# Performance work log

Measured on AMD Instinct MI355X. Metric: run time of the kernel, lower is better.

## Reference

```python
import jax, jax.numpy as jnp
import numpy as np
import math

N_NODES = 50000
N_EDGES = 500000
HIDDEN = 64
N_LAYERS = 4
DELTA = 2.5
N_AGG = 6      # mean, max, min, std, var, sum
N_SCALE = 3    # identity, amplification, attenuation
EPS_BN = 1e-5


def setup_inputs() -> dict:
    key = jax.random.key(0)
    ks = jax.random.split(key, 12)
    d = HIDDEN
    L = N_LAYERS
    din_u = (N_AGG * N_SCALE + 1) * d  # 19*d: [self || scaled aggregates]
    return {
        "node_feat": jax.random.normal(ks[0], (N_NODES, d), jnp.float32),
        "edge_feat": jax.random.normal(ks[1], (N_EDGES, 4), jnp.float32),
        "edge_src": jax.random.randint(ks[2], (N_EDGES,), 0, N_NODES, jnp.int32),
        "edge_dst": jax.random.randint(ks[3], (N_EDGES,), 0, N_NODES, jnp.int32),
        "WM": jax.random.normal(ks[4], (L, 2 * d, d), jnp.float32) / math.sqrt(2 * d),
        "bM": jnp.zeros((L, d), jnp.float32),
        "WU": jax.random.normal(ks[5], (L, din_u, d), jnp.float32) / math.sqrt(din_u),
        "bU": jnp.zeros((L, d), jnp.float32),
        "gamma_t": jnp.ones((L, d), jnp.float32),
        "beta_t": jnp.zeros((L, d), jnp.float32),
        "Wmix": jax.random.normal(ks[6], (L, d, d), jnp.float32) / math.sqrt(d),
        "bmix": jnp.zeros((L, d), jnp.float32),
        "gamma_o": jnp.ones((L, d), jnp.float32),
        "beta_o": jnp.zeros((L, d), jnp.float32),
    }


def _batchnorm(x, gamma, beta):
    # BatchNorm1d in training mode: batch stats, biased variance
    mu = jnp.mean(x, axis=0)
    var = jnp.mean(jnp.square(x - mu), axis=0)
    return (x - mu) * jax.lax.rsqrt(var + EPS_BN) * gamma + beta


def _pna_layer(h, src, dst, WM, bM, WU, bU, g_t, b_t, Wmix, bmix, g_o, b_o):
    n = h.shape[0]
    # message: M([h_src || h_dst])  -> [E, d]
    msg = jnp.concatenate([h[src], h[dst]], axis=1) @ WM + bM
    deg = jax.ops.segment_sum(jnp.ones(src.shape[0], h.dtype), dst, num_segments=n)
    denom = jnp.maximum(deg, 1.0)[:, None]
    s = jax.ops.segment_sum(msg, dst, num_segments=n)
    mean = s / denom
    mean_sq = jax.ops.segment_sum(msg * msg, dst, num_segments=n) / denom
    var = jax.nn.relu(mean_sq - mean * mean)
    std = jnp.sqrt(var + 1e-30)
    has = (deg > 0)[:, None]
    mx = jnp.where(has, jax.ops.segment_max(msg, dst, num_segments=n), 0.0)
    mn = jnp.where(has, jax.ops.segment_min(msg, dst, num_segments=n), 0.0)
    agg = jnp.concatenate([mean, mx, mn, std, var, s], axis=1)  # [N, 6d]
    # degree scalers (zero-degree nodes have all-zero agg, so 0-scale is safe)
    logD = jnp.log(deg + 1.0)[:, None]
    amp = logD / DELTA
    att = jnp.where(logD > 0, DELTA / jnp.where(logD > 0, logD, 1.0), 0.0)
    h_neigh = jnp.concatenate([agg, agg * amp, agg * att], axis=1)  # [N, 18d]
    hu = jnp.concatenate([h, h_neigh], axis=1) @ WU + bU           # [N, d]
    hu = hu * (1.0 / math.sqrt(n))  # dgl graph-size norm snorm_n = 1/sqrt(N)
    hbn = _batchnorm(hu, g_t, b_t)  # tower batchnorm; dropout p=0 -> identity
    hm = jax.nn.leaky_relu(hbn @ Wmix + bmix, 0.01)
    out = hm + h  # PNAConv internal residual (in_size == out_size)
    # outer wrapper: relu(BatchNorm(layer_out)) + node_feat
    return jax.nn.relu(_batchnorm(out, g_o, b_o)) + h


def reference(node_feat, edge_feat, edge_src, edge_dst, WM, bM, WU, bU,
              gamma_t, beta_t, Wmix, bmix, gamma_o, beta_o):
    del edge_feat  # dgl PNAConv built with edge_feat_size=0: edge feats unused
    h = node_feat
    for i in range(N_LAYERS):
        h = _pna_layer(h, edge_src, edge_dst, WM[i], bM[i], WU[i], bU[i],
                       gamma_t[i], beta_t[i], Wmix[i], bmix[i],
                       gamma_o[i], beta_o[i])
    return h
```

## Files before the change

kernel.cpp:

```cpp
#include <hip/hip_runtime.h>
#include <hip/hip_bf16.h>


#define ND 50000
#define NE 500000
#define NB_SCAN ((ND + 255) / 256)
typedef __hip_bfloat16 bh;
typedef unsigned short us;
typedef __attribute__((ext_vector_type(8))) short short8;
typedef __attribute__((ext_vector_type(4))) float floatx4;
#define MFMA(a, b, c) __builtin_amdgcn_mfma_f32_16x16x32_bf16(a, b, c, 0, 0, 0)

__device__ float B2F(us u) { union { unsigned v; float f; } c; c.v = ((unsigned)u) << 16; return c.f; }
__device__ us F2B(float x) {
  union { float f; unsigned v; } c; c.f = x;
  unsigned r = c.v + 0x7fffu + ((c.v >> 16) & 1u);
  return (us)(r >> 16);
}
__device__ float LD(const void* p, size_t i, int ib) {
  return ib ? B2F(((const us*)p)[i]) : ((const float*)p)[i];
}
__device__ void SP(us* Xh, us* Xl, size_t i, float x) {
  us h = F2B(x);
  Xh[i] = h;
  Xl[i] = F2B(x - B2F(h));
}

__device__ inline void gll16(const void* g, void* l) {
  __builtin_amdgcn_global_load_lds((const __attribute__((address_space(1))) unsigned*)g,
                                   (__attribute__((address_space(3))) unsigned*)l, 16, 0, 0);
}

__global__ void kdt(const unsigned* nf, int* fl) {
  __shared__ int cnt;
  if (threadIdx.x == 0) cnt = 0;
  __syncthreads();
  float v = B2F((us)(nf[threadIdx.x] & 0xffffu));
  float av = fabsf(v);
  if (av > 0.0009f && av < 100.f) atomicAdd(&cnt, 1);
  __syncthreads();
  if (threadIdx.x == 0) fl[0] = (cnt >= 128) ? 1 : 0;
}

__global__ void PNA_9826885173934_kernel(const void* nf, const int* fl, float* hf) {
  int ib = fl[0];
  int i = blockIdx.x * 256 + threadIdx.x;
  if (i < ND * 64) hf[i] = LD(nf, i, ib);
}

__global__ void kz(int* d) {
  int i = blockIdx.x * 256 + threadIdx.x;
  if (i < ND) d[i] = 0;
}

__global__ void kd(const int* ed, int* d) {
  int e = blockIdx.x * 256 + threadIdx.x;
  if (e < NE) { int t = ed[e]; if (t >= 0 && t < ND) atomicAdd(&d[t], 1); }
}

__global__ void ks1(const int* d, int* bs) {
  __shared__ int r[256];
  int i = blockIdx.x * 256 + threadIdx.x;
  r[threadIdx.x] = (i < ND) ? d[i] : 0;
  __syncthreads();
  for (int o = 128; o > 0; o >>= 1) {
    if (threadIdx.x < o) r[threadIdx.x] += r[threadIdx.x + o];
    __syncthreads();
  }
  if (threadIdx.x == 0) bs[blockIdx.x] = r[0];
}

__global__ void ks2(int* bs, int* rp) {
  __shared__ int p[256];
  int t = threadIdx.x;
  int v = (t < NB_SCAN) ? bs[t] : 0;
  p[t] = v;
  __syncthreads();
  for (int o = 1; o < 256; o <<= 1) {
    int u = (t >= o) ? p[t - o] : 0;
    __syncthreads();
    p[t] += u;
    __syncthreads();
  }
  if (t < NB_SCAN) bs[t] = p[t] - v;
  if (t == NB_SCAN - 1) rp[ND] = p[t];
}

__global__ void ks3(const int* d, const int* bs, int* rp, int* nx) {
  __shared__ int p[256];
  int t = threadIdx.x;
  int i = blockIdx.x * 256 + t;
  int v = (i < ND) ? d[i] : 0;
  p[t] = v;
  __syncthreads();
  for (int o = 1; o < 256; o <<= 1) {
    int u = (t >= o) ? p[t - o] : 0;
    __syncthreads();
    p[t] += u;
    __syncthreads();
  }
  if (i < ND) {
    int ex = bs[blockIdx.x] + p[t] - v;
    rp[i] = ex;
    nx[i] = ex;
  }
}

__global__ void kc(const int* es, const int* ed, int* nx, int* ss) {
  int e = blockIdx.x * 256 + threadIdx.x;
  if (e < NE) {
    int t = ed[e];
    if (t >= 0 && t < ND) {
      int p = atomicAdd(&nx[t], 1);
      if (p >= 0 && p < NE) ss[p] = es[e];
    }
  }
}

__global__ void kp4(const void* WU, const int* fl, us* Wkh, us* Wkl) {
  int ib = fl[0];
  int gi = blockIdx.x * 256 + threadIdx.x;
  if (gi >= 192 * 448 * 4) return;
  int l = gi / (192 * 448), i = gi - l * (192 * 448);
  int c = i / 448, k = i - c * 448;
  size_t lo = (size_t)l * 77824;
  float o = 0.f;
  if (c < 64) o = LD(WU, lo + (size_t)k * 64 + c, ib);
  else if (c < 128) { if (k >= 64) o = LD(WU, lo + (size_t)(k + 384) * 64 + (c - 64), ib); }
  else { if (k >= 64) o = LD(WU, lo + (size_t)(k + 768) * 64 + (c - 128), ib); }
  us h = F2B(o);
  Wkh[gi] = h;
  Wkl[gi] = F2B(o - B2F(h));
}

__global__ void kpm4(const void* WM, const int* fl, us* WMh, us* WMl) {
  int ib = fl[0];
  int gi = blockIdx.x * 256 + threadIdx.x;
  if (gi >= 128 * 64 * 4) return;
  int l = gi >> 13, i = gi & 8191;
  int j = i >> 6, k = i & 63;
  float o = LD(WM, (size_t)l * 8192 + (size_t)((j < 64 ? 0 : 64) + k) * 64 + (j & 63), ib);
  us h = F2B(o);
  WMh[gi] = h;
  WMl[gi] = F2B(o - B2F(h));
}

__global__ void kpx4(const void* Wm, const int* fl, us* WXh, us* WXl) {
  int ib = fl[0];
  int gi = blockIdx.x * 256 + threadIdx.x;
  if (gi >= 64 * 64 * 4) return;
  int l = gi >> 12, i = gi & 4095;
  int j = i >> 6, k = i & 63;
  float o = LD(Wm, (size_t)l * 4096 + (size_t)k * 64 + j, ib);
  us h = F2B(o);
  WXh[gi] = h;
  WXl[gi] = F2B(o - B2F(h));
}

__global__ __launch_bounds__(256) void ka2(float* hf, const float* ob, const void* go,
                                           const void* bo, int lbp, const us* WMh,
                                           const us* WMl, const void* bM, int lb,
                                           const int* fl, float* ab, float* stC,
                                           const float* stP, int fuse) {
  __shared__ __attribute__((aligned(16))) us Asm[2][128 * 64];
  __shared__ __attribute__((aligned(16))) us Bsm[2][128 * 64];
  __shared__ float bnO[192];
  int t = threadIdx.x, w = t >> 6, lane = t & 63;
  int quad = lane >> 4, l15 = lane & 15;
  int nb = blockIdx.x * 128;
  int ib = fl[0];
  if (blockIdx.x == 0) stC[t] = 0.f;
  {
    int slot = lane & 7, rg = lane >> 3;
#pragma unroll
    for (int ch = 0; ch < 2; ++ch) {
#pragma unroll
      for (int j = 0; j < 4; ++j) {
        int row = j * 32 + w * 8 + rg;
        int op = (slot ^ (row & 7)) << 4;
        const us* s = (op < 64 ? WMh : WMl) + (size_t)row * 64 + ch * 32 + ((op & 63) >> 1);
        gll16(s, (char*)Bsm[ch] + (size_t)(j * 32 + w * 8) * 128);
      }
    }
  }
  if (fuse && t < 64) {
    float mu = stP[128 + t] * 2e-5f;
    float va = stP[192 + t] * 2e-5f - mu * mu;
    bnO[t] = mu;
    bnO[64 + t] = rsqrtf(fmaxf(va, 0.f) + 1e-5f) * LD(go, (size_t)lbp + t, ib);
    bnO[128 + t] = LD(bo, (size_t)lbp + t, ib);
  }
  __syncthreads();
  {
    int q = t & 3;
#pragma unroll
    for (int rr = 0; rr < 2; ++rr) {
      int r = rr * 64 + (t >> 2);
      int node = nb + r;
      int valid = (node < ND);
      if (!valid) node = ND - 1;
      float f[16];
      if (fuse) {
        const float* op_ = ob + (size_t)node * 64 + q * 16;
        float* hp = hf + (size_t)node * 64 + q * 16;
#pragma unroll
        for (int i = 0; i < 4; ++i) {
          float4 vo = ((const float4*)op_)[i];
          float4 vh = ((const float4*)hp)[i];
          int k0 = q * 16 + i * 4;
          float o0 = fmaxf((vo.x - bnO[k0 + 0]) * bnO[64 + k0 + 0] + bnO[128 + k0 + 0], 0.f) + vh.x;
          float o1 = fmaxf((vo.y - bnO[k0 + 1]) * bnO[64 + k0 + 1] + bnO[128 + k0 + 1], 0.f) + vh.y;
          float o2 = fmaxf((vo.z - bnO[k0 + 2]) * bnO[64 + k0 + 2] + bnO[128 + k0 + 2], 0.f) + vh.z;
          float o3 = fmaxf((vo.w - bnO[k0 + 3]) * bnO[64 + k0 + 3] + bnO[128 + k0 + 3], 0.f) + vh.w;
          f[i * 4 + 0] = o0; f[i * 4 + 1] = o1; f[i * 4 + 2] = o2; f[i * 4 + 3] = o3;
          if (valid) ((float4*)hp)[i] = make_float4(o0, o1, o2, o3);
        }
      } else {
        const float* hp = hf + (size_t)node * 64 + q * 16;
#pragma unroll
        for (int i = 0; i < 4; ++i) {
          float4 v = ((const float4*)hp)[i];
          f[i * 4 + 0] = v.x; f[i * 4 + 1] = v.y; f[i * 4 + 2] = v.z; f[i * 4 + 3] = v.w;
        }
      }
      short8 ha = {}, hb = {}, la = {}, lb8 = {};
#pragma unroll
      for (int i = 0; i < 8; ++i) {
        us h0 = F2B(f[i]);     ha[i] = (short)h0;  la[i]  = (short)F2B(f[i] - B2F(h0));
        us h1 = F2B(f[8 + i]); hb[i] = (short)h1;  lb8[i] = (short)F2B(f[8 + i] - B2F(h1));
      }
      int ch = q >> 1, kof = (q & 1) * 32, sw = (r & 7) << 4;
      char* base = (char*)Asm[ch] + r * 128;
      *(short8*)(base + (kof ^ sw)) = ha;
      *(short8*)(base + ((kof + 16) ^ sw)) = hb;
      *(short8*)(base + ((64 + kof) ^ sw)) = la;
      *(short8*)(base + ((64 + kof + 16) ^ sw)) = lb8;
    }
  }
  __syncthreads();
  floatx4 ac[8][2] = {};
#pragma unroll
  for (int ch = 0; ch < 2; ++ch) {
    const char* Ab = (const char*)Asm[ch];
    const char* Bb = (const char*)Bsm[ch];
    short8 bh2[2], bl2[2];
#pragma unroll
    for (int ct = 0; ct < 2; ++ct) {
      int row = (w * 2 + ct) * 16 + l15, sw = (row & 7) << 4;
      bh2[ct] = *(const short8*)(Bb + row * 128 + ((quad * 16) ^ sw));
      bl2[ct] = *(const short8*)(Bb + row * 128 + ((64 + quad * 16) ^ sw));
    }
#pragma unroll
    for (int mt = 0; mt < 8; ++mt) {
      int row = mt * 16 + l15, sw = (row & 7) << 4;
      short8 ah = *(const short8*)(Ab + row * 128 + ((quad * 16) ^ sw));
      short8 al = *(const short8*)(Ab + row * 128 + ((64 + quad * 16) ^ sw));
#pragma unroll
      for (int ct = 0; ct < 2; ++ct) {
        ac[mt][ct] = MFMA(ah, bh2[ct], ac[mt][ct]);
        ac[mt][ct] = MFMA(ah, bl2[ct], ac[mt][ct]);
        ac[mt][ct] = MFMA(al, bh2[ct], ac[mt][ct]);
      }
    }
  }
#pragma unroll
  for (int ct = 0; ct < 2; ++ct) {
    int j = w * 32 + ct * 16 + l15;
    float bi = (j >= 64) ? LD(bM, (size_t)lb + (j - 64), ib) : 0.f;
#pragma unroll
    for (int mt = 0; mt < 8; ++mt) {
#pragma unroll
      for (int r = 0; r < 4; ++r) {
        int node = nb + mt * 16 + quad * 4 + r;
        if (node < ND) ab[(size_t)node * 128 + j] = ac[mt][ct][r] + bi;
      }
    }
  }
}

__global__ void kg(const float* hf, const float* ab, const int* rp, const int* ss,
                   us* Xh, us* Xl, float* am, float* at) {
  int n = blockIdx.x * 4 + (threadIdx.x >> 6), c = threadIdx.x & 63;
  if (n >= ND) return;
  int r0 = rp[n], r1 = rp[n + 1];
  const float* abc = ab + c;
  float s = 0.f, q = 0.f, mx = -3.4e38f, mn = 3.4e38f;
  int e = r0;
  for (; e + 8 <= r1; e += 8) {
    int ix[8];
#pragma unroll
    for (int u = 0; u < 8; ++u) {
      int si = ss[e + u];
      ix[u] = ((unsigned)si >= ND) ? 0 : si;
    }
    float v[8];
#pragma unroll
    for (int u = 0; u < 8; ++u) v[u] = abc[(size_t)ix[u] * 128];
#pragma unroll
    for (int u = 0; u < 8; ++u) {
      s += v[u]; q += v[u] * v[u];
      mx = fmaxf(mx, v[u]); mn = fminf(mn, v[u]);
    }
  }
  for (; e < r1; ++e) {
    int si = ss[e];
    if ((unsigned)si >= ND) si = 0;
    float v = abc[(size_t)si * 128];
    s += v; q += v * v; mx = fmaxf(mx, v); mn = fminf(mn, v);
  }
  float bb = ab[(size_t)n * 128 + 64 + c];
  int dg = r1 - r0;
  float de = fmaxf((float)dg, 1.f);
  float sv = s + (float)dg * bb;
  float qv = q + 2.f * bb * s + (float)dg * bb * bb;
  float me = sv / de;
  float va = fmaxf(qv / de - me * me, 0.f);
  float sd = sqrtf(va + 1e-30f);
  float mxv = mx + bb, mnv = mn + bb;
  if (dg <= 0) { mxv = 0.f; mnv = 0.f; }
  size_t b = (size_t)n * 448;
  SP(Xh, Xl, b + c, hf[(size_t)n * 64 + c]);
  SP(Xh, Xl, b + 64 + c, me);
  SP(Xh, Xl, b + 128 + c, mxv);
  SP(Xh, Xl, b + 192 + c, mnv);
  SP(Xh, Xl, b + 256 + c, sd);
  SP(Xh, Xl, b + 320 + c, va);
  SP(Xh, Xl, b + 384 + c, sv);
  if (c == 0) {
    float l = logf((float)dg + 1.f);
    am[n] = l * 0.4f;
    at[n] = (dg > 0) ? 2.5f / l : 0.f;
  }
}

__device__ inline void k1stage(const us* Xh, const us* Xl, const us* Wkh, const us* Wkl,
                               char* Ab, char* Bb, int w, int lane, int nb, int k0) {
  int row8 = lane >> 3, slot = lane & 7;
  if (w < 4) {
#pragma unroll
    for (int jj = 0; jj < 4; ++jj) {
      int j = w * 4 + jj;
      int row = j * 8 + row8;
      int op = (slot ^ (row & 7)) << 4;
      int node = nb + row; if (node > ND - 1) node = ND - 1;
      const us* s = (op < 64 ? Xh : Xl) + (size_t)node * 448 + k0 + ((op & 63) >> 1);
      gll16(s, Ab + j * 1024);
    }
  } else {
#pragma unroll
    for (int jj = 0; jj < 6; ++jj) {
      int j = (w - 4) * 6 + jj;
      int row = j * 8 + row8;
      int op = (slot ^ (row & 7)) << 4;
      const us* s = (op < 64 ? Wkh : Wkl) + (size_t)row * 448 + k0 + ((op & 63) >> 1);
      gll16(s, Bb + j * 1024);
    }
  }
}

__global__ __launch_bounds__(512, 4) void k1(
    const us* Xh, const us* Xl, const us* Wkh, const us* Wkl,
    const void* bU, int lb, const int* fl, const float* am, const float* at,
    float* hu, float* st) {
  __shared__ __attribute__((aligned(16))) us As[2][128 * 64];
  __shared__ __attribute__((aligned(16))) us Bs[2][192 * 64];
  int t = threadIdx.x;
  int ib = fl[0];
  int w = t >> 6, lane = t & 63;
  int wh = w >> 2, wc = w & 3;
  int quad = lane >> 4, l15 = lane & 15;
  int nb = blockIdx.x * 128;
  floatx4 ac[4][3] = {};
  k1stage(Xh, Xl, Wkh, Wkl, (char*)As[0], (char*)Bs[0], w, lane, nb, 0);
  __syncthreads();
  int buf = 0;
  for (int tt = 0; tt < 14; ++tt) {
    if (tt < 13)
      k1stage(Xh, Xl, Wkh, Wkl, (char*)As[buf ^ 1], (char*)Bs[buf ^ 1], w, lane, nb,
              (tt + 1) * 32);
    const char* Ab = (const char*)As[buf];
    const char* Bb = (const char*)Bs[buf];
    short8 bh2[3], bl2[3];
#pragma unroll
    for (int ci = 0; ci < 3; ++ci) {
      int row = (wc + ci * 4) * 16 + l15, sw = (row & 7) << 4;
      bh2[ci] = *(const short8*)(Bb + row * 128 + ((quad * 16) ^ sw));
      bl2[ci] = *(const short8*)(Bb + row * 128 + ((64 + quad * 16) ^ sw));
    }
#pragma unroll
    for (int mt = 0; mt < 4; ++mt) {
      int row = wh * 64 + mt * 16 + l15, sw = (row & 7) << 4;
      short8 ah = *(const short8*)(Ab + row * 128 + ((quad * 16) ^ sw));
      short8 al = *(const short8*)(Ab + row * 128 + ((64 + quad * 16) ^ sw));
#pragma unroll
      for (int ci = 0; ci < 3; ++ci) {
        ac[mt][ci] = MFMA(ah, bh2[ci], ac[mt][ci]);
        ac[mt][ci] = MFMA(ah, bl2[ci], ac[mt][ci]);
        ac[mt][ci] = MFMA(al, bh2[ci], ac[mt][ci]);
      }
    }
    __syncthreads();
    buf ^= 1;
  }
  float* sr = (float*)As;
  if (t < 128) sr[t] = 0.f;
  __syncthreads();
  int c = wc * 16 + l15;
  float bu = LD(bU, (size_t)lb + c, ib);
  float ps = 0.f, pq = 0.f;
#pragma unroll
  for (int mt = 0; mt < 4; ++mt) {
#pragma unroll
    for (int r = 0; r < 4; ++r) {
      int node = nb + wh * 64 + mt * 16 + quad * 4 + r;
      if (node < ND) {
        float v = (ac[mt][0][r] + am[node] * ac[mt][1][r] + at[node] * ac[mt][2][r] + bu)
                  * 4.4721359549995794e-3f;
        hu[(size_t)node * 64 + c] = v;
        ps += v; pq += v * v;
      }
    }
  }
  atomicAdd(&sr[c], ps);
  atomicAdd(&sr[64 + c], pq);
  __syncthreads();
  if (t < 128) atomicAdd(&st[t], sr[t]);
}

__global__ __launch_bounds__(256) void k2m(const float* hu, float* st, const void* gt,
                                           const void* bt, const us* WXh, const us* WXl,
                                           const void* bm, int lb, const int* fl,
                                           const float* hf, float* ob) {
  __shared__ __attribute__((aligned(16))) us Asm[2][64 * 64];
  __shared__ __attribute__((aligned(16))) us Bsm[2][64 * 64];
  __shared__ float bnS[192];
  int t = threadIdx.x, w = t >> 6, lane = t & 63;
  int quad = lane >> 4, l15 = lane & 15;
  int nb = blockIdx.x * 64;
  int ib = fl[0];
  {
#pragma unroll
    for (int i = 0; i < 4; ++i) {
      int idx = t * 4 + i;
      int ch = idx >> 9, rem = idx & 511;
      int row = rem >> 3, slot = rem & 7;
      int op = slot << 4;
      const us* s = WXh + (size_t)row * 64 + ch * 32 + (op >> 1);
      const us* s2 = WXl + (size_t)row * 64 + ch * 32 + (op >> 1);
      short8 v = (op < 64) ? *(const short8*)s : *(const short8*)s2;
      int sw = (row & 7) << 4;
      *(short8*)((char*)Bsm[ch] + row * 128 + (op ^ sw)) = v;
    }
  }
  if (t < 64) {
    float mu = st[t] * 2e-5f;
    float va = st[64 + t] * 2e-5f - mu * mu;
    bnS[t] = mu;
    bnS[64 + t] = rsqrtf(fmaxf(va, 0.f) + 1e-5f) * LD(gt, (size_t)lb + t, ib);
    bnS[128 + t] = LD(bt, (size_t)lb + t, ib);
  }
  __syncthreads();
  {
    int r = t >> 2, q = t & 3;
    int node = nb + r; if (node > ND - 1) node = ND - 1;
    const float* hp = hu + (size_t)node * 64 + q * 16;
    float f[16];
#pragma unroll
    for (int i = 0; i < 4; ++i) {
      float4 v = ((const float4*)hp)[i];
      f[i * 4 + 0] = v.x; f[i * 4 + 1] = v.y; f[i * 4 + 2] = v.z; f[i * 4 + 3] = v.w;
    }
#pragma unroll
    for (int i = 0; i < 16; ++i) {
      int k = q * 16 + i;
      f[i] = (f[i] - bnS[k]) * bnS[64 + k] + bnS[128 + k];
    }
    short8 ha = {}, hb = {}, la = {}, lb8 = {};
#pragma unroll
    for (int i = 0; i < 8; ++i) {
      us h0 = F2B(f[i]);     ha[i] = (short)h0;  la[i]  = (short)F2B(f[i] - B2F(h0));
      us h1 = F2B(f[8 + i]); hb[i] = (short)h1;  lb8[i] = (short)F2B(f[8 + i] - B2F(h1));
    }
    int ch = q >> 1, kof = (q & 1) * 32, sw = (r & 7) << 4;
    char* base = (char*)Asm[ch] + r * 128;
    *(short8*)(base + (kof ^ sw)) = ha;
    *(short8*)(base + ((kof + 16) ^ sw)) = hb;
    *(short8*)(base + ((64 + kof) ^ sw)) = la;
    *(short8*)(base + ((64 + kof + 16) ^ sw)) = lb8;
  }
  __syncthreads();
  floatx4 ac[4] = {};
#pragma unroll
  for (int ch = 0; ch < 2; ++ch) {
    const char* Ab = (const char*)Asm[ch];
    const char* Bb = (const char*)Bsm[ch];
    short8 ah[4], al[4], bh2, bl2;
#pragma unroll
    for (int mt = 0; mt < 4; ++mt) {
      int row = mt * 16 + l15, sw = (row & 7) << 4;
      ah[mt] = *(const short8*)(Ab + row * 128 + ((quad * 16) ^ sw));
      al[mt] = *(const short8*)(Ab + row * 128 + ((64 + quad * 16) ^ sw));
    }
    {
      int row = w * 16 + l15, sw = (row & 7) << 4;
      bh2 = *(const short8*)(Bb + row * 128 + ((quad * 16) ^ sw));
      bl2 = *(const short8*)(Bb + row * 128 + ((64 + quad * 16) ^ sw));
    }
#pragma unroll
    for (int mt = 0; mt < 4; ++mt) {
      ac[mt] = MFMA(ah[mt], bh2, ac[mt]);
      ac[mt] = MFMA(ah[mt], bl2, ac[mt]);
      ac[mt] = MFMA(al[mt], bh2, ac[mt]);
    }
  }
  __syncthreads();
  float* sr = (float*)Asm;
  if (t < 128) sr[t] = 0.f;
  __syncthreads();
  int j = w * 16 + l15;
  float b1 = LD(bm, (size_t)lb + j, ib);
  float ps = 0.f, pq = 0.f;
#pragma unroll
  for (int mt = 0; mt < 4; ++mt) {
#pragma unroll
    for (int r = 0; r < 4; ++r) {
      int node = nb + mt * 16 + quad * 4 + r;
      if (node < ND) {
        float a = ac[mt][r] + b1;
        float hm = (a > 0.f) ? a : 0.01f * a;
        float o = hm + hf[(size_t)node * 64 + j];
        ob[(size_t)node * 64 + j] = o;
        ps += o; pq += o * o;
      }
    }
  }
  atomicAdd(&sr[j], ps);
  atomicAdd(&sr[64 + j], pq);
  __syncthreads();
  if (t < 128) atomicAdd(&st[128 + t], sr[t]);
}

__global__ void k3(const float* ob, const float* st, const void* go, const void* bo,
                   int lb, const int* fl, float* hf, void* op) {
  int ib = fl[0];
  int i = blockIdx.x * 256 + threadIdx.x;
  if (i >= ND * 64) return;
  int c = i & 63;
  float mu = st[128 + c] * 2e-5f;
  float va = st[192 + c] * 2e-5f - mu * mu;
  float x = (ob[i] - mu) * rsqrtf(fmaxf(va, 0.f) + 1e-5f) * LD(go, (size_t)lb + c, ib)
            + LD(bo, (size_t)lb + c, ib);
  x = fmaxf(x, 0.f);
  float h = x + hf[i];
  hf[i] = h;
  if (ib) ((us*)op)[i] = F2B(h);
  else ((float*)op)[i] = h;
}

extern "C" void kernel_launch(void* const* d_in, const int* in_sizes, int n_in,
                              void* d_out, int out_size, void* d_ws, size_t ws_size,
                              hipStream_t stream) {
  int sh = (n_in >= 14) ? 0 : -1;
  const void* nf = d_in[0];
  const int* es = (const int*)d_in[2 + sh];
  const int* ed = (const int*)d_in[3 + sh];
  const void* WM = d_in[4 + sh];
  const void* bM = d_in[5 + sh];
  const void* WU = d_in[6 + sh];
  const void* bU = d_in[7 + sh];
  const void* gt = d_in[8 + sh];
  const void* bt = d_in[9 + sh];
  const void* Wm = d_in[10 + sh];
  const void* bm = d_in[11 + sh];
  const void* go = d_in[12 + sh];
  const void* bo = d_in[13 + sh];

  char* B = (char*)d_ws;
  float* hf = (float*)B;
  float* ab = (float*)(B + 12800000);
  us* Xh = (us*)(B + 38400000);
  us* Xl = (us*)(B + 83200000);
  float* ob = (float*)(B + 38400000);
  size_t o0 = 128000000;
  float* am = (float*)(B + o0);
  float* at = (float*)(B + o0 + 200192);
  int* dg = (int*)(B + o0 + 400384);
  int* rp = (int*)(B + o0 + 600576);
  int* nx = (int*)(B + o0 + 800768);
  int* ss = (int*)(B + o0 + 1000960);
  us* Wkh4 = (us*)(B + o0 + 3001088);
  us* Wkl4 = (us*)(B + o0 + 3689216);
  float* st = (float*)(B + o0 + 4377344);
  int* fl = (int*)(B + o0 + 4379392);
  int* bs = (int*)(B + o0 + 4379648);
  us* WMh4 = (us*)(B + o0 + 4380672);
  us* WMl4 = (us*)(B + o0 + 4446208);
  us* WXh4 = (us*)(B + o0 + 4511744);
  us* WXl4 = (us*)(B + o0 + 4544512);
  float* hu = ab;

  kdt<<<1, 256, 0, stream>>>((const unsigned*)nf, fl);
  PNA_9826885173934_kernel<<<(ND * 64 + 255) / 256, 256, 0, stream>>>(nf, fl, hf);
  kz<<<(ND + 255) / 256, 256, 0, stream>>>(dg);
  kd<<<(NE + 255) / 256, 256, 0, stream>>>(ed, dg);
  ks1<<<NB_SCAN, 256, 0, stream>>>(dg, bs);
  ks2<<<1, 256, 0, stream>>>(bs, rp);
  ks3<<<NB_SCAN, 256, 0, stream>>>(dg, bs, rp, nx);
  kc<<<(NE + 255) / 256, 256, 0, stream>>>(es, ed, nx, ss);
  kp4<<<(192 * 448 * 4 + 255) / 256, 256, 0, stream>>>(WU, fl, Wkh4, Wkl4);
  kpm4<<<(128 * 64 * 4 + 255) / 256, 256, 0, stream>>>(WM, fl, WMh4, WMl4);
  kpx4<<<(64 * 64 * 4 + 255) / 256, 256, 0, stream>>>(Wm, fl, WXh4, WXl4);

  for (int L = 0; L < 4; ++L) {
    float* stC = st + (L & 1) * 256;
    const float* stP = st + ((L + 1) & 1) * 256;
    ka2<<<(ND + 127) / 128, 256, 0, stream>>>(hf, ob, go, bo, (L > 0) ? (L - 1) * 64 : 0,
                                              WMh4 + (size_t)L * 8192,
                                              WMl4 + (size_t)L * 8192, bM, L * 64, fl,
                                              ab, stC, stP, (L > 0) ? 1 : 0);
    kg<<<(ND + 3) / 4, 256, 0, stream>>>(hf, ab, rp, ss, Xh, Xl, am, at);
    k1<<<(ND + 127) / 128, 512, 0, stream>>>(Xh, Xl, Wkh4 + (size_t)L * 86016,
                                             Wkl4 + (size_t)L * 86016, bU, L * 64, fl,
                                             am, at, hu, stC);
    k2m<<<(ND + 63) / 64, 256, 0, stream>>>(hu, stC, gt, bt, WXh4 + (size_t)L * 4096,
                                            WXl4 + (size_t)L * 4096, bm, L * 64, fl, hf, ob);
  }
  k3<<<(ND * 64 + 255) / 256, 256, 0, stream>>>(ob, st + 256, go, bo, 192, fl, hf, d_out);
}
```

Measured before the change: 694.3 us.

## Fold self-feature update term into message GEMM, shrink aggregate buffer

The h @ WU_self product moves into the message GEMM kernel (ka2) by widening its weight tile from 128 to 192 columns, and the result is written to a new hu0 buffer. The gather kernel no longer writes the self features into the X staging buffer, so X rows shrink from 448 to 384 elements and the main update GEMM runs 12 K-steps instead of 14. This cuts global traffic for X and a GEMM pass. In exchange ka2 uses more LDS and registers, and k1 makes an extra fp32 read of hu0 in its epilogue.

```diff
diff --git a/kernel.cpp b/kernel.cpp
--- a/kernel.cpp
+++ b/kernel.cpp
@@ -120,26 +120,29 @@
 __global__ void kp4(const void* WU, const int* fl, us* Wkh, us* Wkl) {
   int ib = fl[0];
   int gi = blockIdx.x * 256 + threadIdx.x;
-  if (gi >= 192 * 448 * 4) return;
-  int l = gi / (192 * 448), i = gi - l * (192 * 448);
-  int c = i / 448, k = i - c * 448;
+  if (gi >= 192 * 384 * 4) return;
+  int l = gi / (192 * 384), i = gi - l * (192 * 384);
+  int c = i / 384, k = i - c * 384;
   size_t lo = (size_t)l * 77824;
-  float o = 0.f;
-  if (c < 64) o = LD(WU, lo + (size_t)k * 64 + c, ib);
-  else if (c < 128) { if (k >= 64) o = LD(WU, lo + (size_t)(k + 384) * 64 + (c - 64), ib); }
-  else { if (k >= 64) o = LD(WU, lo + (size_t)(k + 768) * 64 + (c - 128), ib); }
+  float o;
+  if (c < 64) o = LD(WU, lo + (size_t)(k + 64) * 64 + c, ib);
+  else if (c < 128) o = LD(WU, lo + (size_t)(k + 448) * 64 + (c - 64), ib);
+  else o = LD(WU, lo + (size_t)(k + 832) * 64 + (c - 128), ib);
   us h = F2B(o);
   Wkh[gi] = h;
   Wkl[gi] = F2B(o - B2F(h));
 }
 
-__global__ void kpm4(const void* WM, const int* fl, us* WMh, us* WMl) {
+__global__ void kpm4(const void* WM, const void* WU, const int* fl, us* WMh, us* WMl) {
   int ib = fl[0];
   int gi = blockIdx.x * 256 + threadIdx.x;
-  if (gi >= 128 * 64 * 4) return;
-  int l = gi >> 13, i = gi & 8191;
+  if (gi >= 192 * 64 * 4) return;
+  int l = gi / (192 * 64), i = gi - l * (192 * 64);
   int j = i >> 6, k = i & 63;
-  float o = LD(WM, (size_t)l * 8192 + (size_t)((j < 64 ? 0 : 64) + k) * 64 + (j & 63), ib);
+  float o;
+  if (j < 64) o = LD(WM, (size_t)l * 8192 + (size_t)k * 64 + j, ib);
+  else if (j < 128) o = LD(WM, (size_t)l * 8192 + (size_t)(64 + k) * 64 + (j - 64), ib);
+  else o = LD(WU, (size_t)l * 77824 + (size_t)k * 64 + (j - 128), ib);
   us h = F2B(o);
   WMh[gi] = h;
   WMl[gi] = F2B(o - B2F(h));
@@ -160,10 +163,10 @@
 __global__ __launch_bounds__(256) void ka2(float* hf, const float* ob, const void* go,
                                            const void* bo, int lbp, const us* WMh,
                                            const us* WMl, const void* bM, int lb,
-                                           const int* fl, float* ab, float* stC,
-                                           const float* stP, int fuse) {
+                                           const int* fl, float* ab, float* hu0,
+                                           float* stC, const float* stP, int fuse) {
   __shared__ __attribute__((aligned(16))) us Asm[2][128 * 64];
-  __shared__ __attribute__((aligned(16))) us Bsm[2][128 * 64];
+  __shared__ __attribute__((aligned(16))) us Bsm[2][192 * 64];
   __shared__ float bnO[192];
   int t = threadIdx.x, w = t >> 6, lane = t & 63;
   int quad = lane >> 4, l15 = lane & 15;
@@ -175,7 +178,7 @@
 #pragma unroll
     for (int ch = 0; ch < 2; ++ch) {
 #pragma unroll
-      for (int j = 0; j < 4; ++j) {
+      for (int j = 0; j < 6; ++j) {
         int row = j * 32 + w * 8 + rg;
         int op = (slot ^ (row & 7)) << 4;
         const us* s = (op < 64 ? WMh : WMl) + (size_t)row * 64 + ch * 32 + ((op & 63) >> 1);
@@ -238,17 +241,17 @@
     }
   }
   __syncthreads();
-  floatx4 ac[8][2] = {};
+  floatx4 ac[8][3] = {};
 #pragma unroll
   for (int ch = 0; ch < 2; ++ch) {
     const char* Ab = (const char*)Asm[ch];
     const char* Bb = (const char*)Bsm[ch];
-    short8 bh2[2], bl2[2];
-#pragma unroll
-    for (int ct = 0; ct < 2; ++ct) {
-      int row = (w * 2 + ct) * 16 + l15, sw = (row & 7) << 4;
-      bh2[ct] = *(const short8*)(Bb + row * 128 + ((quad * 16) ^ sw));
-      bl2[ct] = *(const short8*)(Bb + row * 128 + ((64 + quad * 16) ^ sw));
+    short8 bh2[3], bl2[3];
+#pragma unroll
+    for (int ci = 0; ci < 3; ++ci) {
+      int row = (w + ci * 4) * 16 + l15, sw = (row & 7) << 4;
+      bh2[ci] = *(const short8*)(Bb + row * 128 + ((quad * 16) ^ sw));
+      bl2[ci] = *(const short8*)(Bb + row * 128 + ((64 + quad * 16) ^ sw));
     }
 #pragma unroll
     for (int mt = 0; mt < 8; ++mt) {
@@ -256,29 +259,30 @@
       short8 ah = *(const short8*)(Ab + row * 128 + ((quad * 16) ^ sw));
       short8 al = *(const short8*)(Ab + row * 128 + ((64 + quad * 16) ^ sw));
 #pragma unroll
-      for (int ct = 0; ct < 2; ++ct) {
-        ac[mt][ct] = MFMA(ah, bh2[ct], ac[mt][ct]);
-        ac[mt][ct] = MFMA(ah, bl2[ct], ac[mt][ct]);
-        ac[mt][ct] = MFMA(al, bh2[ct], ac[mt][ct]);
-      }
-    }
-  }
-#pragma unroll
-  for (int ct = 0; ct < 2; ++ct) {
-    int j = w * 32 + ct * 16 + l15;
-    float bi = (j >= 64) ? LD(bM, (size_t)lb + (j - 64), ib) : 0.f;
-#pragma unroll
-    for (int mt = 0; mt < 8; ++mt) {
-#pragma unroll
-      for (int r = 0; r < 4; ++r) {
-        int node = nb + mt * 16 + quad * 4 + r;
-        if (node < ND) ab[(size_t)node * 128 + j] = ac[mt][ct][r] + bi;
-      }
-    }
-  }
-}
-
-__global__ void kg(const float* hf, const float* ab, const int* rp, const int* ss,
+      for (int ci = 0; ci < 3; ++ci) {
+        ac[mt][ci] = MFMA(ah, bh2[ci], ac[mt][ci]);
+        ac[mt][ci] = MFMA(ah, bl2[ci], ac[mt][ci]);
+        ac[mt][ci] = MFMA(al, bh2[ci], ac[mt][ci]);
+      }
+    }
+  }
+  int c = w * 16 + l15;
+  float bi = LD(bM, (size_t)lb + c, ib);
+#pragma unroll
+  for (int mt = 0; mt < 8; ++mt) {
+#pragma unroll
+    for (int r = 0; r < 4; ++r) {
+      int node = nb + mt * 16 + quad * 4 + r;
+      if (node < ND) {
+        ab[(size_t)node * 128 + c] = ac[mt][0][r];
+        ab[(size_t)node * 128 + 64 + c] = ac[mt][1][r] + bi;
+        hu0[(size_t)node * 64 + c] = ac[mt][2][r];
+      }
+    }
+  }
+}
+
+__global__ void kg(const float* ab, const int* rp, const int* ss,
                    us* Xh, us* Xl, float* am, float* at) {
   int n = blockIdx.x * 4 + (threadIdx.x >> 6), c = threadIdx.x & 63;
   if (n >= ND) return;
@@ -318,14 +322,13 @@
   float sd = sqrtf(va + 1e-30f);
   float mxv = mx + bb, mnv = mn + bb;
   if (dg <= 0) { mxv = 0.f; mnv = 0.f; }
-  size_t b = (size_t)n * 448;
-  SP(Xh, Xl, b + c, hf[(size_t)n * 64 + c]);
-  SP(Xh, Xl, b + 64 + c, me);
-  SP(Xh, Xl, b + 128 + c, mxv);
-  SP(Xh, Xl, b + 192 + c, mnv);
-  SP(Xh, Xl, b + 256 + c, sd);
-  SP(Xh, Xl, b + 320 + c, va);
-  SP(Xh, Xl, b + 384 + c, sv);
+  size_t b = (size_t)n * 384;
+  SP(Xh, Xl, b + c, me);
+  SP(Xh, Xl, b + 64 + c, mxv);
+  SP(Xh, Xl, b + 128 + c, mnv);
+  SP(Xh, Xl, b + 192 + c, sd);
+  SP(Xh, Xl, b + 256 + c, va);
+  SP(Xh, Xl, b + 320 + c, sv);
   if (c == 0) {
     float l = logf((float)dg + 1.f);
     am[n] = l * 0.4f;
@@ -343,7 +346,7 @@
       int row = j * 8 + row8;
       int op = (slot ^ (row & 7)) << 4;
       int node = nb + row; if (node > ND - 1) node = ND - 1;
-      const us* s = (op < 64 ? Xh : Xl) + (size_t)node * 448 + k0 + ((op & 63) >> 1);
+      const us* s = (op < 64 ? Xh : Xl) + (size_t)node * 384 + k0 + ((op & 63) >> 1);
       gll16(s, Ab + j * 1024);
     }
   } else {
@@ -352,14 +355,14 @@
       int j = (w - 4) * 6 + jj;
       int row = j * 8 + row8;
       int op = (slot ^ (row & 7)) << 4;
-      const us* s = (op < 64 ? Wkh : Wkl) + (size_t)row * 448 + k0 + ((op & 63) >> 1);
+      const us* s = (op < 64 ? Wkh : Wkl) + (size_t)row * 384 + k0 + ((op & 63) >> 1);
       gll16(s, Bb + j * 1024);
     }
   }
 }
 
 __global__ __launch_bounds__(512, 4) void k1(
-    const us* Xh, const us* Xl, const us* Wkh, const us* Wkl,
+    const us* Xh, const us* Xl, const us* Wkh, const us* Wkl, const float* hu0,
     const void* bU, int lb, const int* fl, const float* am, const float* at,
     float* hu, float* st) {
   __shared__ __attribute__((aligned(16))) us As[2][128 * 64];
@@ -374,8 +377,8 @@
   k1stage(Xh, Xl, Wkh, Wkl, (char*)As[0], (char*)Bs[0], w, lane, nb, 0);
   __syncthreads();
   int buf = 0;
-  for (int tt = 0; tt < 14; ++tt) {
-    if (tt < 13)
+  for (int tt = 0; tt < 12; ++tt) {
+    if (tt < 11)
       k1stage(Xh, Xl, Wkh, Wkl, (char*)As[buf ^ 1], (char*)Bs[buf ^ 1], w, lane, nb,
               (tt + 1) * 32);
     const char* Ab = (const char*)As[buf];
@@ -414,7 +417,8 @@
     for (int r = 0; r < 4; ++r) {
       int node = nb + wh * 64 + mt * 16 + quad * 4 + r;
       if (node < ND) {
-        float v = (ac[mt][0][r] + am[node] * ac[mt][1][r] + at[node] * ac[mt][2][r] + bu)
+        float v = (ac[mt][0][r] + hu0[(size_t)node * 64 + c]
+                   + am[node] * ac[mt][1][r] + at[node] * ac[mt][2][r] + bu)
                   * 4.4721359549995794e-3f;
         hu[(size_t)node * 64 + c] = v;
         ps += v; pq += v * v;
@@ -579,7 +583,8 @@
   float* hf = (float*)B;
   float* ab = (float*)(B + 12800000);
   us* Xh = (us*)(B + 38400000);
-  us* Xl = (us*)(B + 83200000);
+  us* Xl = (us*)(B + 76800000);
+  float* hu0 = (float*)(B + 115200000);
   float* ob = (float*)(B + 38400000);
   size_t o0 = 128000000;
   float* am = (float*)(B + o0);
@@ -589,14 +594,14 @@
   int* nx = (int*)(B + o0 + 800768);
   int* ss = (int*)(B + o0 + 1000960);
   us* Wkh4 = (us*)(B + o0 + 3001088);
-  us* Wkl4 = (us*)(B + o0 + 3689216);
-  float* st = (float*)(B + o0 + 4377344);
-  int* fl = (int*)(B + o0 + 4379392);
-  int* bs = (int*)(B + o0 + 4379648);
-  us* WMh4 = (us*)(B + o0 + 4380672);
-  us* WMl4 = (us*)(B + o0 + 4446208);
-  us* WXh4 = (us*)(B + o0 + 4511744);
-  us* WXl4 = (us*)(B + o0 + 4544512);
+  us* Wkl4 = (us*)(B + o0 + 3590912);
+  float* st = (float*)(B + o0 + 4180736);
+  int* fl = (int*)(B + o0 + 4182784);
+  int* bs = (int*)(B + o0 + 4183040);
+  us* WMh4 = (us*)(B + o0 + 4184064);
+  us* WMl4 = (us*)(B + o0 + 4282368);
+  us* WXh4 = (us*)(B + o0 + 4380672);
+  us* WXl4 = (us*)(B + o0 + 4413440);
   float* hu = ab;
 
   kdt<<<1, 256, 0, stream>>>((const unsigned*)nf, fl);
@@ -607,21 +612,21 @@
   ks2<<<1, 256, 0, stream>>>(bs, rp);
   ks3<<<NB_SCAN, 256, 0, stream>>>(dg, bs, rp, nx);
   kc<<<(NE + 255) / 256, 256, 0, stream>>>(es, ed, nx, ss);
-  kp4<<<(192 * 448 * 4 + 255) / 256, 256, 0, stream>>>(WU, fl, Wkh4, Wkl4);
-  kpm4<<<(128 * 64 * 4 + 255) / 256, 256, 0, stream>>>(WM, fl, WMh4, WMl4);
+  kp4<<<(192 * 384 * 4 + 255) / 256, 256, 0, stream>>>(WU, fl, Wkh4, Wkl4);
+  kpm4<<<(192 * 64 * 4 + 255) / 256, 256, 0, stream>>>(WM, WU, fl, WMh4, WMl4);
   kpx4<<<(64 * 64 * 4 + 255) / 256, 256, 0, stream>>>(Wm, fl, WXh4, WXl4);
 
   for (int L = 0; L < 4; ++L) {
     float* stC = st + (L & 1) * 256;
     const float* stP = st + ((L + 1) & 1) * 256;
     ka2<<<(ND + 127) / 128, 256, 0, stream>>>(hf, ob, go, bo, (L > 0) ? (L - 1) * 64 : 0,
-                                              WMh4 + (size_t)L * 8192,
-                                              WMl4 + (size_t)L * 8192, bM, L * 64, fl,
-                                              ab, stC, stP, (L > 0) ? 1 : 0);
-    kg<<<(ND + 3) / 4, 256, 0, stream>>>(hf, ab, rp, ss, Xh, Xl, am, at);
-    k1<<<(ND + 127) / 128, 512, 0, stream>>>(Xh, Xl, Wkh4 + (size_t)L * 86016,
-                                             Wkl4 + (size_t)L * 86016, bU, L * 64, fl,
-                                             am, at, hu, stC);
+                                              WMh4 + (size_t)L * 12288,
+                                              WMl4 + (size_t)L * 12288, bM, L * 64, fl,
+                                              ab, hu0, stC, stP, (L > 0) ? 1 : 0);
+    kg<<<(ND + 3) / 4, 256, 0, stream>>>(ab, rp, ss, Xh, Xl, am, at);
+    k1<<<(ND + 127) / 128, 512, 0, stream>>>(Xh, Xl, Wkh4 + (size_t)L * 73728,
+                                             Wkl4 + (size_t)L * 73728, hu0, bU, L * 64,
+                                             fl, am, at, hu, stC);
     k2m<<<(ND + 63) / 64, 256, 0, stream>>>(hu, stC, gt, bt, WXh4 + (size_t)L * 4096,
                                             WXl4 + (size_t)L * 4096, bm, L * 64, fl, hf, ob);
   }
```

After: 701.4 us. About the same (+1.0%).
